# Kernel tuning notes

Hardware: AMD Instinct MI355X
Metric: run time of the kernel (lower is better)

Reference implementation:

```python
import jax, jax.numpy as jnp
import numpy as np

R_CUT = 10.0  # init arg r_cut


def _per_mol(pos, T, eneg, node_attrs, an, q_tot, eidx, hardness, cov_radii):
    # pos [N,3], T [N,E], eneg [N], node_attrs [N,num_el], an [N] int,
    # q_tot scalar, eidx [2,E] int
    N = pos.shape[0]
    E = T.shape[1]
    dtype = pos.dtype
    sqrt_pi = jnp.sqrt(jnp.pi).astype(dtype)
    sqrt_2 = jnp.sqrt(2.0).astype(dtype)
    eye = jnp.eye(N, dtype=dtype)
    # pairwise distances; +eye makes the (masked-out) diagonal sqrt-safe
    diff = pos[:, None, :] - pos[None, :, :]
    d = jnp.sqrt(jnp.sum(diff * diff, axis=-1) + eye)  # [N,N]
    r = cov_radii[an]                                   # [N]
    sigma = r * r
    gamma = jnp.sqrt(sigma[:, None] + sigma[None, :])   # [N,N]
    diag_vals = hardness[jnp.argmax(node_attrs, axis=-1)] + 1.0 / (sqrt_pi * r)
    A = jax.scipy.special.erf(d / (sqrt_2 * gamma)) / d * (1.0 - eye) + jnp.diag(diag_vals)
    # per-edge cutoff diagonal: 1/cos(pi*r/(2*r_cut)) - 1
    e0, e1 = eidx[0], eidx[1]
    edge_d = jnp.sqrt(jnp.sum((pos[e0] - pos[e1]) ** 2, axis=-1))  # [E]
    cut = 1.0 / jnp.cos(jnp.pi * edge_d / (2.0 * R_CUT)) - 1.0
    Ap = T.T @ A @ T + jnp.diag(cut)                    # [E,E]
    # augment with charge-conservation row/col of ones
    ones_col = jnp.ones((E, 1), dtype=dtype)
    ones_row = jnp.ones((1, E + 1), dtype=dtype)
    Aaug = jnp.concatenate([jnp.concatenate([Ap, ones_col], axis=1), ones_row], axis=0)
    b = jnp.concatenate([-(T.T @ eneg), q_tot[None]])   # [E+1]
    x = jnp.linalg.solve(Aaug, b)[:-1]                  # [E] split charges
    return T @ x                                        # [N] atomic partial charges


def setup_inputs() -> dict:
    key = jax.random.key(0)
    B, N, E, NUM_EL, NZ = 256, 64, 512, 10, 119
    ks = jax.random.split(key, 10)
    positions = jax.random.normal(ks[0], (B, N, 3), dtype=jnp.float32)
    T = jax.random.normal(ks[1], (B, N, E), dtype=jnp.float32)
    eneg = jax.random.normal(ks[2], (B, N), dtype=jnp.float32)
    node_attrs = jax.random.normal(ks[3], (B, N, NUM_EL), dtype=jnp.float32)
    total_charge = jax.random.normal(ks[4], (B,), dtype=jnp.float32)
    atomic_numbers = jax.random.randint(ks[5], (B, N), 1, 100)
    e0 = jax.random.randint(ks[6], (B, E), 0, N)
    off = jax.random.randint(ks[7], (B, E), 1, N)
    edge_index = jnp.stack([e0, (e0 + off) % N], axis=1)  # [B,2,E], distinct endpoints
    hardness = jax.random.uniform(ks[8], (NUM_EL,), dtype=jnp.float32)
    cov_radii = 0.3 + 2.2 * jax.random.uniform(ks[9], (NZ,), dtype=jnp.float32)
    p = jnp.zeros((1,), dtype=jnp.float32)  # only used for .device in torch
    return dict(positions=positions, T=T, eneg=eneg, node_attrs=node_attrs,
                total_charge=total_charge, p=p, hardness=hardness,
                cov_radii=cov_radii, atomic_numbers=atomic_numbers,
                edge_index=edge_index)


def reference(positions, T, eneg, node_attrs, total_charge, p, hardness,
              cov_radii, atomic_numbers, edge_index):
    charges = jax.vmap(_per_mol, in_axes=(0, 0, 0, 0, 0, 0, 0, None, None))(
        positions, T, eneg, node_attrs, atomic_numbers, total_charge,
        edge_index, hardness, cov_radii)  # [B,N]
    return charges.reshape(-1)  # concat over molecules, as in the torch loop
```

## Files before the change

kernel.cpp:

```cpp
#include <hip/hip_runtime.h>
#include <math.h>

#define SQRT_PI 1.7724538509055160273
#define SQRT_2  1.4142135623730950488
#define PI_OVER_2RC 0.15707963267948966

typedef double dbl4 __attribute__((ext_vector_type(4)));


__device__ __forceinline__ double bcast64(double v, int lane) {
    union { double d; unsigned int u[2]; } a, r;
    a.d = v;
    r.u[0] = __builtin_amdgcn_readlane(a.u[0], lane);
    r.u[1] = __builtin_amdgcn_readlane(a.u[1], lane);
    return r.d;
}

__device__ __forceinline__ double a_entry(int i, int j, const double* posd,
                                          const double* sig, const double* dg) {
    if (i == j) return dg[i];
    double dx = posd[3*i+0]-posd[3*j+0];
    double dy = posd[3*i+1]-posd[3*j+1];
    double dz = posd[3*i+2]-posd[3*j+2];
    double d  = sqrt(dx*dx+dy*dy+dz*dz);
    double g  = sqrt(sig[i]+sig[j]);
    return erf(d/(SQRT_2*g))/d;
}

__device__ __forceinline__ dbl4 mfma64(int cS, double xv, double yv, dbl4 acc) {
    return cS ? __builtin_amdgcn_mfma_f64_16x16x4f64(yv, xv, acc, 0, 0, 0)
              : __builtin_amdgcn_mfma_f64_16x16x4f64(xv, yv, acc, 0, 0, 0);
}

__global__ __launch_bounds__(64)
void k0_probe(double* __restrict__ fl)
{
    const int l = threadIdx.x;
    const int kl = l >> 4, ml = l & 15;
    const double af1 = (double)(l + 1),  bf1 = (double)(l + 65);
    const double af2 = (double)(1 + ((l*7 + 3) % 61));
    const double bf2 = (double)(2 + ((l*13 + 5) % 53));
    dbl4 c1 = {0.0,0.0,0.0,0.0}, c2 = {0.0,0.0,0.0,0.0};
    c1 = __builtin_amdgcn_mfma_f64_16x16x4f64(af1, bf1, c1, 0, 0, 0);
    c2 = __builtin_amdgcn_mfma_f64_16x16x4f64(af2, bf2, c2, 0, 0, 0);
    int best = -1;
    for (int h = 0; h < 32; ++h) {
        if (best >= 0) break;
        const int cS = h >> 4, cA = (h >> 3) & 1, cB = (h >> 2) & 1, cD = h & 3;
        bool ok = true;
        #pragma unroll
        for (int r = 0; r < 4; ++r) {
            int row, col;
            const int v0 = 4*kl + r, v1 = kl + 4*r;
            if (cD == 0)      { row = v0; col = ml; }
            else if (cD == 1) { row = v1; col = ml; }
            else if (cD == 2) { row = ml; col = v0; }
            else              { row = ml; col = v1; }
            double r1 = 0.0, r2 = 0.0;
            #pragma unroll
            for (int k = 0; k < 4; ++k) {
                const int la = cA ? (row*4 + k) : (row + 16*k);
                const int lb = cB ? (col*4 + k) : (col + 16*k);
                if (cS == 0) {
                    r1 += (double)(la + 1) * (double)(lb + 65);
                    r2 += (double)(1 + ((la*7+3) % 61)) * (double)(2 + ((lb*13+5) % 53));
                } else {
                    r1 += (double)(lb + 1) * (double)(la + 65);
                    r2 += (double)(1 + ((lb*7+3) % 61)) * (double)(2 + ((la*13+5) % 53));
                }
            }
            if (c1[r] != r1 || c2[r] != r2) ok = false;
        }
        if (__ballot(ok) == ~0ull) best = h;
    }
    if (l == 0) {
        fl[0] = (best >= 0) ? 1.0 : 0.0;
        fl[1] = (double)((best >= 0) ? (best >> 4)      : 0);
        fl[2] = (double)((best >= 0) ? ((best >> 3) & 1) : 0);
        fl[3] = (double)((best >= 0) ? ((best >> 2) & 1) : 0);
        fl[4] = (double)((best >= 0) ? (best & 3)        : 0);
    }
}

__global__ __launch_bounds__(1024)
void k_fused(const float* __restrict__ pos, const float* __restrict__ T,
             const int* __restrict__ eidx, const float* __restrict__ nattr,
             const float* __restrict__ eneg, const float* __restrict__ qtot,
             const float* __restrict__ hard, const float* __restrict__ covr,
             const int* __restrict__ an, const double* __restrict__ flq,
             float* __restrict__ outp)
{
    const int m = blockIdx.x, tid = threadIdx.x;
    const int jl = tid & 63;
    const int rg = tid >> 6;
    const int kl = jl >> 4, ml = jl & 15;

    __shared__ double R[2*64*66];
    __shared__ double AB[64*65];
    __shared__ double w_sl[512];
    __shared__ double posd[192], sig_s[64], dg_s[64], eneg_s[64];
    __shared__ double t0a_s[64], t0b_s[64], ga_s[64], gb_s[64];
    __shared__ double ua_s[64], ub_s[64], sa_s[64], sb_s[64];
    __shared__ double dinv_s[64], dvec_s[64];
    __shared__ double lam_sh, sw_sh;

    double* const Ta = R;
    double* const Tb = R + 64*66;
    double* const SB = R;
    double* const Pm = R + 64*66;

    const int cS = (int)flq[1], cA = (int)flq[2], cB = (int)flq[3], cD = (int)flq[4];
    const int aRow = cA ? (jl >> 2) : ml;
    const int aK   = cA ? (jl & 3)  : kl;
    const int bRow = cB ? (jl >> 2) : ml;
    const int bK   = cB ? (jl & 3)  : kl;
    int drow[4], dcol[4];
    #pragma unroll
    for (int r = 0; r < 4; ++r) {
        const int v0 = 4*kl + r, v1 = kl + 4*r;
        if (cD == 0)      { drow[r] = v0; dcol[r] = ml; }
        else if (cD == 1) { drow[r] = v1; dcol[r] = ml; }
        else if (cD == 2) { drow[r] = ml; dcol[r] = v0; }
        else              { drow[r] = ml; dcol[r] = v1; }
    }

    const float* Tm = T + (size_t)m*64*512;
    const int srow = tid >> 4, sc4 = (tid & 15) * 4;

    float4 v = *(const float4*)&Tm[srow*512 + sc4];

    if (tid < 64) {
        posd[3*tid+0] = (double)pos[(m*64+tid)*3+0];
        posd[3*tid+1] = (double)pos[(m*64+tid)*3+1];
        posd[3*tid+2] = (double)pos[(m*64+tid)*3+2];
        double r = (double)covr[an[m*64+tid]];
        sig_s[tid] = r*r;
        const float* np_ = nattr + (size_t)(m*64+tid)*10;
        float best = np_[0]; int bi = 0;
        #pragma unroll
        for (int k = 1; k < 10; ++k) { float vv = np_[k]; if (vv > best) { best = vv; bi = k; } }
        dg_s[tid] = (double)hard[bi] + 1.0/(SQRT_PI*r);
    } else if (tid < 128) {
        int ll = tid - 64;
        eneg_s[ll] = (double)eneg[m*64 + ll];
    }
    __syncthreads();

    if (tid < 512) {
        const int a0 = eidx[(size_t)m*1024 + tid];
        const int a1 = eidx[(size_t)m*1024 + 512 + tid];
        double dx = posd[3*a0+0]-posd[3*a1+0];
        double dy = posd[3*a0+1]-posd[3*a1+1];
        double dz = posd[3*a0+2]-posd[3*a1+2];
        double d  = sqrt(dx*dx+dy*dy+dz*dz);
        w_sl[tid] = 1.0 / (1.0/cos(PI_OVER_2RC*d) - 1.0);
    }
    __syncthreads();

    if (tid < 64) {
        double s = 0.0;
        #pragma unroll
        for (int c = 0; c < 8; ++c) s += w_sl[c*64 + tid];
        #pragma unroll
        for (int off = 32; off > 0; off >>= 1) s += __shfl_down(s, off);
        if (tid == 0) sw_sh = s;
    }

    const int tp = rg >> 2, tq = rg & 3;
    const double* ta_b = &Ta[(size_t)(tp*16 + aRow)*66 + aK];
    const double* tb_b = &Tb[(size_t)(tq*16 + bRow)*66 + bK];
    dbl4 vacc = {0.0, 0.0, 0.0, 0.0};
    double t0b_p = 0.0;
    double areg[4];

    #pragma unroll
    for (int cc = 0; cc < 8; ++cc) {
        __syncthreads();
        const double w0 = w_sl[cc*64 + sc4+0];
        const double w1 = w_sl[cc*64 + sc4+1];
        const double w2 = w_sl[cc*64 + sc4+2];
        const double w3 = w_sl[cc*64 + sc4+3];
        const double d0 = (double)v.x, d1 = (double)v.y;
        const double d2 = (double)v.z, d3 = (double)v.w;
        {
            double2 p0; p0.x = d0; p0.y = d1;
            double2 p1; p1.x = d2; p1.y = d3;
            *(double2*)&Ta[srow*66 + sc4]     = p0;
            *(double2*)&Ta[srow*66 + sc4 + 2] = p1;
            double2 q0; q0.x = w0*d0; q0.y = w1*d1;
            double2 q1; q1.x = w2*d2; q1.y = w3*d3;
            *(double2*)&Tb[srow*66 + sc4]     = q0;
            *(double2*)&Tb[srow*66 + sc4 + 2] = q1;
        }
        t0b_p += d0*w0 + d1*w1 + d2*w2 + d3*w3;
        if (cc < 7) v = *(const float4*)&Tm[srow*512 + (cc+1)*64 + sc4];
        __syncthreads();
        if (cc < 4) {
            const int i = rg + 16*cc;
            double av = a_entry(i, jl, posd, sig_s, dg_s);
            areg[cc] = av;
            AB[i*65 + jl] = av;
        }
        #pragma unroll
        for (int kk = 0; kk < 16; ++kk)
            vacc = mfma64(cS, ta_b[kk*4], tb_b[kk*4], vacc);
    }
    __syncthreads();

    #pragma unroll
    for (int r = 0; r < 4; ++r)
        SB[(tp*16 + drow[r])*66 + tq*16 + dcol[r]] = vacc[r];
    {
        double t = t0b_p;
        t += __shfl_down(t, 8, 16);
        t += __shfl_down(t, 4, 16);
        t += __shfl_down(t, 2, 16);
        t += __shfl_down(t, 1, 16);
        if ((tid & 15) == 0) t0b_s[tid >> 4] = t;
    }
    __syncthreads();

    {
        const int c16 = tid & 15, row16 = tid >> 4;
        double a = 0.0;
        #pragma unroll
        for (int kk = 0; kk < 4; ++kk)
            a += SB[row16*66 + 4*c16 + kk] * eneg_s[4*c16 + kk];
        a += __shfl_down(a, 8, 16);
        a += __shfl_down(a, 4, 16);
        a += __shfl_down(a, 2, 16);
        a += __shfl_down(a, 1, 16);
        if (c16 == 0) t0a_s[row16] = -a;
    }
    __syncthreads();

    {
        double ra[4], rb[4];
        const double ta = t0a_s[jl], tb = t0b_s[jl];
        #pragma unroll
        for (int p = 0; p < 4; ++p) { ra[p] = areg[p]*ta; rb[p] = areg[p]*tb; }
        #pragma unroll
        for (int off = 32; off > 0; off >>= 1) {
            #pragma unroll
            for (int p = 0; p < 4; ++p) {
                ra[p] += __shfl_down(ra[p], off);
                rb[p] += __shfl_down(rb[p], off);
            }
        }
        if (jl == 0) {
            #pragma unroll
            for (int p = 0; p < 4; ++p) { ga_s[rg+16*p] = ra[p]; gb_s[rg+16*p] = rb[p]; }
        }
    }
    __syncthreads();

    {
        const double* xb = &AB[(size_t)(tp*16 + aRow)*65 + aK];
        const double* yb = &SB[(size_t)bK*66 + tq*16 + bRow];
        dbl4 pacc = {0.0, 0.0, 0.0, 0.0};
        #pragma unroll
        for (int kk = 0; kk < 16; ++kk)
            pacc = mfma64(cS, xb[kk*4], yb[kk*264], pacc);
        #pragma unroll
        for (int r = 0; r < 4; ++r)
            Pm[(tp*16 + drow[r])*66 + tq*16 + dcol[r]] = pacc[r];
    }
    __syncthreads();

    {
        dbl4 macc;
        #pragma unroll
        for (int r = 0; r < 4; ++r)
            macc[r] = AB[(tp*16 + drow[r])*65 + tq*16 + dcol[r]];
        const double* xb = &Pm[(size_t)(tp*16 + aRow)*66 + aK];
        const double* yb = &AB[(size_t)bK*65 + tq*16 + bRow];
        #pragma unroll
        for (int kk = 0; kk < 16; ++kk)
            macc = mfma64(cS, xb[kk*4], yb[kk*260], macc);
        __syncthreads();
        #pragma unroll
        for (int r = 0; r < 4; ++r)
            AB[(tp*16 + drow[r])*65 + tq*16 + dcol[r]] = macc[r];
    }
    __syncthreads();

    for (int pb = 0; pb < 4; ++pb) {
        const int kb = pb*16;
        if (tid < 64) {
            const int i = tid;
            double pr[16];
            #pragma unroll
            for (int c = 0; c < 16; ++c) pr[c] = AB[i*65 + kb + c];
            #pragma unroll
            for (int c = 0; c < 16; ++c) {
                const int k = kb + c;
                const double Dk = bcast64(pr[c], k);
                const double di = 1.0 / Dk;
                if (i == k) { dinv_s[k] = di; dvec_s[k] = Dk; }
                const double lik = pr[c] * di;
                #pragma unroll
                for (int j = c+1; j < 16; ++j) {
                    const double mkj = bcast64(pr[j], k);
                    if (i > k) pr[j] -= lik * mkj;
                }
                if (i > k) pr[c] = lik;
            }
            #pragma unroll
            for (int c = 0; c < 16; ++c) AB[i*65 + kb + c] = pr[c];
        }
        __syncthreads();
        const int lim = kb + 16;
        if (lim < 64) {
            double tacc[4] = {0.0, 0.0, 0.0, 0.0};
            #pragma unroll 4
            for (int c = 0; c < 16; ++c) {
                double lbv = AB[jl*65 + kb + c] * dvec_s[kb + c];
                #pragma unroll
                for (int p = 0; p < 4; ++p)
                    tacc[p] += AB[(rg+16*p)*65 + kb + c] * lbv;
            }
            if (jl >= lim) {
                #pragma unroll
                for (int p = 0; p < 4; ++p) {
                    int i = rg + 16*p;
                    if (i >= lim) AB[i*65 + jl] -= tacc[p];
                }
            }
        }
        __syncthreads();
    }

    if (tid < 64) {
        const int i = tid;
        double ha = ga_s[i], hb = gb_s[i];
        #pragma unroll
        for (int j = 0; j < 63; ++j) {
            double xa = bcast64(ha, j), xb = bcast64(hb, j);
            double lij = (i > j) ? AB[i*65+j] : 0.0;
            ha -= lij*xa; hb -= lij*xb;
        }
        double di = dinv_s[i];
        ha *= di; hb *= di;
        #pragma unroll
        for (int j = 63; j > 0; --j) {
            double xa = bcast64(ha, j), xb = bcast64(hb, j);
            double lji = (i < j) ? AB[j*65+i] : 0.0;
            ha -= lji*xa; hb -= lji*xb;
        }
        ua_s[i] = ha; ub_s[i] = hb;
    }
    __syncthreads();

    {
        double ra[4], rb[4];
        const double uaj = ua_s[jl], ubj = ub_s[jl];
        #pragma unroll
        for (int p = 0; p < 4; ++p) { ra[p] = areg[p]*uaj; rb[p] = areg[p]*ubj; }
        #pragma unroll
        for (int off = 32; off > 0; off >>= 1) {
            #pragma unroll
            for (int p = 0; p < 4; ++p) {
                ra[p] += __shfl_down(ra[p], off);
                rb[p] += __shfl_down(rb[p], off);
            }
        }
        if (jl == 0) {
            #pragma unroll
            for (int p = 0; p < 4; ++p) {
                sa_s[rg + 16*p] = ra[p];
                sb_s[rg + 16*p] = rb[p];
            }
        }
    }
    __syncthreads();

    if (tid < 64) {
        double d1 = (eneg_s[tid] + sa_s[tid]) * t0b_s[tid];
        double d2 = sb_s[tid] * t0b_s[tid];
        #pragma unroll
        for (int off = 32; off > 0; off >>= 1) {
            d1 += __shfl_down(d1, off);
            d2 += __shfl_down(d2, off);
        }
        if (tid == 0) {
            double sY = -d1;
            double sZ = sw_sh - d2;
            lam_sh = ((double)qtot[m] - sY) / (1.0 - sZ);
        }
    }
    __syncthreads();
    if (tid < 64)
        outp[m*64 + tid] = (float)(ua_s[tid] - lam_sh*ub_s[tid]);
}

extern "C" void kernel_launch(void* const* d_in, const int* in_sizes, int n_in,
                              void* d_out, int out_size, void* d_ws, size_t ws_size,
                              hipStream_t stream) {
    const float* pos  = (const float*)d_in[0];
    const float* T    = (const float*)d_in[1];
    const float* eneg = (const float*)d_in[2];
    const float* nat  = (const float*)d_in[3];
    const float* qt   = (const float*)d_in[4];
    const float* hard = (const float*)d_in[6];
    const float* covr = (const float*)d_in[7];
    const int*   an   = (const int*)d_in[8];
    const int*   eidx = (const int*)d_in[9];
    float* outp = (float*)d_out;
    (void)n_in; (void)out_size; (void)ws_size;

    const int B = in_sizes[4];
    double* ws = (double*)d_ws;

    k0_probe<<<dim3(1), dim3(64), 0, stream>>>(ws);
    k_fused<<<dim3(B), dim3(1024), 0, stream>>>(pos, T, eidx, nat, eneg, qt,
                                                hard, covr, an, ws, outp);
}
```

Measured before the change: 169.1 us.

## Fuse MFMA layout probe, exploit Gram symmetry, and software-pipeline MFMA operand loads

Removes the separate probe kernel and runs the MFMA lane-layout detection inside each block, in parallel across four waves while other waves load per-atom data. The T^T·W·T Gram product is now computed only for its 10 upper-triangular 16x16 tiles. Waves are assigned to split the k-range of those tiles, with mirrored writes and a second accumulation pass. MFMA operand loads are double-buffered in registers, and a couple of barriers are merged or removed. This adds an extra sync and shared-memory read-modify-write, plus redundant probe work in every block.

```diff
diff --git a/kernel.cpp b/kernel.cpp
--- a/kernel.cpp
+++ b/kernel.cpp
@@ -6,7 +6,6 @@
 #define PI_OVER_2RC 0.15707963267948966
 
 typedef double dbl4 __attribute__((ext_vector_type(4)));
-
 
 __device__ __forceinline__ double bcast64(double v, int lane) {
     union { double d; unsigned int u[2]; } a, r;
@@ -32,63 +31,12 @@
               : __builtin_amdgcn_mfma_f64_16x16x4f64(xv, yv, acc, 0, 0, 0);
 }
 
-__global__ __launch_bounds__(64)
-void k0_probe(double* __restrict__ fl)
-{
-    const int l = threadIdx.x;
-    const int kl = l >> 4, ml = l & 15;
-    const double af1 = (double)(l + 1),  bf1 = (double)(l + 65);
-    const double af2 = (double)(1 + ((l*7 + 3) % 61));
-    const double bf2 = (double)(2 + ((l*13 + 5) % 53));
-    dbl4 c1 = {0.0,0.0,0.0,0.0}, c2 = {0.0,0.0,0.0,0.0};
-    c1 = __builtin_amdgcn_mfma_f64_16x16x4f64(af1, bf1, c1, 0, 0, 0);
-    c2 = __builtin_amdgcn_mfma_f64_16x16x4f64(af2, bf2, c2, 0, 0, 0);
-    int best = -1;
-    for (int h = 0; h < 32; ++h) {
-        if (best >= 0) break;
-        const int cS = h >> 4, cA = (h >> 3) & 1, cB = (h >> 2) & 1, cD = h & 3;
-        bool ok = true;
-        #pragma unroll
-        for (int r = 0; r < 4; ++r) {
-            int row, col;
-            const int v0 = 4*kl + r, v1 = kl + 4*r;
-            if (cD == 0)      { row = v0; col = ml; }
-            else if (cD == 1) { row = v1; col = ml; }
-            else if (cD == 2) { row = ml; col = v0; }
-            else              { row = ml; col = v1; }
-            double r1 = 0.0, r2 = 0.0;
-            #pragma unroll
-            for (int k = 0; k < 4; ++k) {
-                const int la = cA ? (row*4 + k) : (row + 16*k);
-                const int lb = cB ? (col*4 + k) : (col + 16*k);
-                if (cS == 0) {
-                    r1 += (double)(la + 1) * (double)(lb + 65);
-                    r2 += (double)(1 + ((la*7+3) % 61)) * (double)(2 + ((lb*13+5) % 53));
-                } else {
-                    r1 += (double)(lb + 1) * (double)(la + 65);
-                    r2 += (double)(1 + ((lb*7+3) % 61)) * (double)(2 + ((la*13+5) % 53));
-                }
-            }
-            if (c1[r] != r1 || c2[r] != r2) ok = false;
-        }
-        if (__ballot(ok) == ~0ull) best = h;
-    }
-    if (l == 0) {
-        fl[0] = (best >= 0) ? 1.0 : 0.0;
-        fl[1] = (double)((best >= 0) ? (best >> 4)      : 0);
-        fl[2] = (double)((best >= 0) ? ((best >> 3) & 1) : 0);
-        fl[3] = (double)((best >= 0) ? ((best >> 2) & 1) : 0);
-        fl[4] = (double)((best >= 0) ? (best & 3)        : 0);
-    }
-}
-
-__global__ __launch_bounds__(1024)
+__global__ __launch_bounds__(1024, 4)
 void k_fused(const float* __restrict__ pos, const float* __restrict__ T,
              const int* __restrict__ eidx, const float* __restrict__ nattr,
              const float* __restrict__ eneg, const float* __restrict__ qtot,
              const float* __restrict__ hard, const float* __restrict__ covr,
-             const int* __restrict__ an, const double* __restrict__ flq,
-             float* __restrict__ outp)
+             const int* __restrict__ an, float* __restrict__ outp)
 {
     const int m = blockIdx.x, tid = threadIdx.x;
     const int jl = tid & 63;
@@ -103,13 +51,77 @@
     __shared__ double ua_s[64], ub_s[64], sa_s[64], sb_s[64];
     __shared__ double dinv_s[64], dvec_s[64];
     __shared__ double lam_sh, sw_sh;
+    __shared__ int fl_w[4];
 
     double* const Ta = R;
     double* const Tb = R + 64*66;
     double* const SB = R;
     double* const Pm = R + 64*66;
 
-    const int cS = (int)flq[1], cA = (int)flq[2], cB = (int)flq[3], cD = (int)flq[4];
+    const float* Tm = T + (size_t)m*64*512;
+    const int srow = tid >> 4, sc4 = (tid & 15) * 4;
+
+    float4 v = *(const float4*)&Tm[srow*512 + sc4];
+
+    if (rg < 4) {
+        const double af1 = (double)(jl + 1),  bf1 = (double)(jl + 65);
+        const double af2 = (double)(1 + ((jl*7 + 3) % 61));
+        const double bf2 = (double)(2 + ((jl*13 + 5) % 53));
+        dbl4 c1 = {0.0,0.0,0.0,0.0}, c2 = {0.0,0.0,0.0,0.0};
+        c1 = __builtin_amdgcn_mfma_f64_16x16x4f64(af1, bf1, c1, 0, 0, 0);
+        c2 = __builtin_amdgcn_mfma_f64_16x16x4f64(af2, bf2, c2, 0, 0, 0);
+        int myh = -1;
+        for (int hh = 0; hh < 8; ++hh) {
+            const int h = rg*8 + hh;
+            const int pS = h >> 4, pA = (h >> 3) & 1, pB = (h >> 2) & 1, pD = h & 3;
+            bool ok = true;
+            #pragma unroll
+            for (int r = 0; r < 4; ++r) {
+                int row, col;
+                const int v0 = 4*kl + r, v1 = kl + 4*r;
+                if (pD == 0)      { row = v0; col = ml; }
+                else if (pD == 1) { row = v1; col = ml; }
+                else if (pD == 2) { row = ml; col = v0; }
+                else              { row = ml; col = v1; }
+                double r1 = 0.0, r2 = 0.0;
+                #pragma unroll
+                for (int k = 0; k < 4; ++k) {
+                    const int la = pA ? (row*4 + k) : (row + 16*k);
+                    const int lb = pB ? (col*4 + k) : (col + 16*k);
+                    if (pS == 0) {
+                        r1 += (double)(la + 1) * (double)(lb + 65);
+                        r2 += (double)(1 + ((la*7+3) % 61)) * (double)(2 + ((lb*13+5) % 53));
+                    } else {
+                        r1 += (double)(lb + 1) * (double)(la + 65);
+                        r2 += (double)(1 + ((lb*7+3) % 61)) * (double)(2 + ((la*13+5) % 53));
+                    }
+                }
+                if (c1[r] != r1 || c2[r] != r2) ok = false;
+            }
+            if (__ballot(ok) == ~0ull) myh = h;
+        }
+        if (jl == 0) fl_w[rg] = myh;
+    } else if (tid >= 256 && tid < 320) {
+        const int at = tid - 256;
+        posd[3*at+0] = (double)pos[(m*64+at)*3+0];
+        posd[3*at+1] = (double)pos[(m*64+at)*3+1];
+        posd[3*at+2] = (double)pos[(m*64+at)*3+2];
+        double r = (double)covr[an[m*64+at]];
+        sig_s[at] = r*r;
+        const float* np_ = nattr + (size_t)(m*64+at)*10;
+        float best = np_[0]; int bi = 0;
+        #pragma unroll
+        for (int k = 1; k < 10; ++k) { float vv = np_[k]; if (vv > best) { best = vv; bi = k; } }
+        dg_s[at] = (double)hard[bi] + 1.0/(SQRT_PI*r);
+    } else if (tid >= 320 && tid < 384) {
+        const int at = tid - 320;
+        eneg_s[at] = (double)eneg[m*64 + at];
+    }
+    __syncthreads();
+
+    int hbest = max(max(fl_w[0], fl_w[1]), max(fl_w[2], fl_w[3]));
+    if (hbest < 0) hbest = 1;
+    const int cS = hbest >> 4, cA = (hbest >> 3) & 1, cB = (hbest >> 2) & 1, cD = hbest & 3;
     const int aRow = cA ? (jl >> 2) : ml;
     const int aK   = cA ? (jl & 3)  : kl;
     const int bRow = cB ? (jl >> 2) : ml;
@@ -124,28 +136,6 @@
         else              { drow[r] = ml; dcol[r] = v1; }
     }
 
-    const float* Tm = T + (size_t)m*64*512;
-    const int srow = tid >> 4, sc4 = (tid & 15) * 4;
-
-    float4 v = *(const float4*)&Tm[srow*512 + sc4];
-
-    if (tid < 64) {
-        posd[3*tid+0] = (double)pos[(m*64+tid)*3+0];
-        posd[3*tid+1] = (double)pos[(m*64+tid)*3+1];
-        posd[3*tid+2] = (double)pos[(m*64+tid)*3+2];
-        double r = (double)covr[an[m*64+tid]];
-        sig_s[tid] = r*r;
-        const float* np_ = nattr + (size_t)(m*64+tid)*10;
-        float best = np_[0]; int bi = 0;
-        #pragma unroll
-        for (int k = 1; k < 10; ++k) { float vv = np_[k]; if (vv > best) { best = vv; bi = k; } }
-        dg_s[tid] = (double)hard[bi] + 1.0/(SQRT_PI*r);
-    } else if (tid < 128) {
-        int ll = tid - 64;
-        eneg_s[ll] = (double)eneg[m*64 + ll];
-    }
-    __syncthreads();
-
     if (tid < 512) {
         const int a0 = eidx[(size_t)m*1024 + tid];
         const int a1 = eidx[(size_t)m*1024 + 512 + tid];
@@ -155,18 +145,13 @@
         double d  = sqrt(dx*dx+dy*dy+dz*dz);
         w_sl[tid] = 1.0 / (1.0/cos(PI_OVER_2RC*d) - 1.0);
     }
-    __syncthreads();
-
-    if (tid < 64) {
-        double s = 0.0;
-        #pragma unroll
-        for (int c = 0; c < 8; ++c) s += w_sl[c*64 + tid];
-        #pragma unroll
-        for (int off = 32; off > 0; off >>= 1) s += __shfl_down(s, off);
-        if (tid == 0) sw_sh = s;
-    }
-
-    const int tp = rg >> 2, tq = rg & 3;
+
+    const int TP_[10] = {0,1,1,2,2,2,3,3,3,3};
+    const int TQ_[10] = {0,0,1,0,1,2,0,1,2,3};
+    const int WT[16] = {0,4,4,5,5,1,6,6,7,7,2,8,8,9,9,3};
+    const int WM[16] = {0,1,2,1,2,0,1,2,1,2,0,1,2,1,2,0};
+    const int myt = WT[rg], wm = WM[rg];
+    const int tp = TP_[myt], tq = TQ_[myt];
     const double* ta_b = &Ta[(size_t)(tp*16 + aRow)*66 + aK];
     const double* tb_b = &Tb[(size_t)(tq*16 + bRow)*66 + bK];
     dbl4 vacc = {0.0, 0.0, 0.0, 0.0};
@@ -195,21 +180,55 @@
         t0b_p += d0*w0 + d1*w1 + d2*w2 + d3*w3;
         if (cc < 7) v = *(const float4*)&Tm[srow*512 + (cc+1)*64 + sc4];
         __syncthreads();
+        if (cc == 0 && tid >= 128 && tid < 192) {
+            const int ll = tid - 128;
+            double s = 0.0;
+            #pragma unroll
+            for (int c = 0; c < 8; ++c) s += w_sl[c*64 + ll];
+            #pragma unroll
+            for (int off = 32; off > 0; off >>= 1) s += __shfl_down(s, off);
+            if (ll == 0) sw_sh = s;
+        }
         if (cc < 4) {
             const int i = rg + 16*cc;
             double av = a_entry(i, jl, posd, sig_s, dg_s);
             areg[cc] = av;
             AB[i*65 + jl] = av;
         }
-        #pragma unroll
-        for (int kk = 0; kk < 16; ++kk)
-            vacc = mfma64(cS, ta_b[kk*4], tb_b[kk*4], vacc);
-    }
-    __syncthreads();
-
-    #pragma unroll
-    for (int r = 0; r < 4; ++r)
-        SB[(tp*16 + drow[r])*66 + tq*16 + dcol[r]] = vacc[r];
+        const bool act = (wm == 0) || (wm == 1 ? ((cc & 1) == 0) : ((cc & 1) == 1));
+        if (act) {
+            double xc[4], yc[4];
+            #pragma unroll
+            for (int q = 0; q < 4; ++q) { xc[q] = ta_b[q*4]; yc[q] = tb_b[q*4]; }
+            #pragma unroll
+            for (int kb = 0; kb < 4; ++kb) {
+                double xn[4], yn[4];
+                if (kb < 3) {
+                    #pragma unroll
+                    for (int q = 0; q < 4; ++q) {
+                        xn[q] = ta_b[(kb*4+4+q)*4];
+                        yn[q] = tb_b[(kb*4+4+q)*4];
+                    }
+                }
+                #pragma unroll
+                for (int q = 0; q < 4; ++q) vacc = mfma64(cS, xc[q], yc[q], vacc);
+                if (kb < 3) {
+                    #pragma unroll
+                    for (int q = 0; q < 4; ++q) { xc[q] = xn[q]; yc[q] = yn[q]; }
+                }
+            }
+        }
+    }
+    __syncthreads();
+
+    if (wm != 2) {
+        #pragma unroll
+        for (int r = 0; r < 4; ++r) {
+            const int ri = tp*16 + drow[r], cj = tq*16 + dcol[r];
+            SB[ri*66 + cj] = vacc[r];
+            if (tp != tq) SB[cj*66 + ri] = vacc[r];
+        }
+    }
     {
         double t = t0b_p;
         t += __shfl_down(t, 8, 16);
@@ -219,8 +238,45 @@
         if ((tid & 15) == 0) t0b_s[tid >> 4] = t;
     }
     __syncthreads();
-
+    if (wm == 2) {
+        #pragma unroll
+        for (int r = 0; r < 4; ++r) {
+            const int ri = tp*16 + drow[r], cj = tq*16 + dcol[r];
+            const double vv = vacc[r];
+            SB[ri*66 + cj] += vv;
+            if (tp != tq) SB[cj*66 + ri] += vv;
+        }
+    }
+    __syncthreads();
+
+    const int ti = rg >> 2, tj = rg & 3;
     {
+        const double* xb = &AB[(size_t)(ti*16 + aRow)*65 + aK];
+        const double* yb = &SB[(size_t)bK*66 + tj*16 + bRow];
+        dbl4 pacc = {0.0, 0.0, 0.0, 0.0};
+        double xc[4], yc[4];
+        #pragma unroll
+        for (int q = 0; q < 4; ++q) { xc[q] = xb[q*4]; yc[q] = yb[q*264]; }
+        #pragma unroll
+        for (int kb = 0; kb < 4; ++kb) {
+            double xn[4], yn[4];
+            if (kb < 3) {
+                #pragma unroll
+                for (int q = 0; q < 4; ++q) {
+                    xn[q] = xb[(kb*4+4+q)*4];
+                    yn[q] = yb[(size_t)(kb*4+4+q)*264];
+                }
+            }
+            #pragma unroll
+            for (int q = 0; q < 4; ++q) pacc = mfma64(cS, xc[q], yc[q], pacc);
+            if (kb < 3) {
+                #pragma unroll
+                for (int q = 0; q < 4; ++q) { xc[q] = xn[q]; yc[q] = yn[q]; }
+            }
+        }
+        #pragma unroll
+        for (int r = 0; r < 4; ++r)
+            Pm[(ti*16 + drow[r])*66 + tj*16 + dcol[r]] = pacc[r];
         const int c16 = tid & 15, row16 = tid >> 4;
         double a = 0.0;
         #pragma unroll
@@ -235,52 +291,54 @@
     __syncthreads();
 
     {
-        double ra[4], rb[4];
-        const double ta = t0a_s[jl], tb = t0b_s[jl];
-        #pragma unroll
-        for (int p = 0; p < 4; ++p) { ra[p] = areg[p]*ta; rb[p] = areg[p]*tb; }
-        #pragma unroll
-        for (int off = 32; off > 0; off >>= 1) {
-            #pragma unroll
-            for (int p = 0; p < 4; ++p) {
-                ra[p] += __shfl_down(ra[p], off);
-                rb[p] += __shfl_down(rb[p], off);
-            }
-        }
-        if (jl == 0) {
-            #pragma unroll
-            for (int p = 0; p < 4; ++p) { ga_s[rg+16*p] = ra[p]; gb_s[rg+16*p] = rb[p]; }
-        }
-    }
-    __syncthreads();
-
-    {
-        const double* xb = &AB[(size_t)(tp*16 + aRow)*65 + aK];
-        const double* yb = &SB[(size_t)bK*66 + tq*16 + bRow];
-        dbl4 pacc = {0.0, 0.0, 0.0, 0.0};
-        #pragma unroll
-        for (int kk = 0; kk < 16; ++kk)
-            pacc = mfma64(cS, xb[kk*4], yb[kk*264], pacc);
+        dbl4 macc;
         #pragma unroll
         for (int r = 0; r < 4; ++r)
-            Pm[(tp*16 + drow[r])*66 + tq*16 + dcol[r]] = pacc[r];
-    }
-    __syncthreads();
-
-    {
-        dbl4 macc;
+            macc[r] = AB[(ti*16 + drow[r])*65 + tj*16 + dcol[r]];
+        const double* xb = &Pm[(size_t)(ti*16 + aRow)*66 + aK];
+        const double* yb = &AB[(size_t)bK*65 + tj*16 + bRow];
+        double xc[4], yc[4];
+        #pragma unroll
+        for (int q = 0; q < 4; ++q) { xc[q] = xb[q*4]; yc[q] = yb[q*260]; }
+        #pragma unroll
+        for (int kb = 0; kb < 4; ++kb) {
+            double xn[4], yn[4];
+            if (kb < 3) {
+                #pragma unroll
+                for (int q = 0; q < 4; ++q) {
+                    xn[q] = xb[(kb*4+4+q)*4];
+                    yn[q] = yb[(size_t)(kb*4+4+q)*260];
+                }
+            }
+            #pragma unroll
+            for (int q = 0; q < 4; ++q) macc = mfma64(cS, xc[q], yc[q], macc);
+            if (kb < 3) {
+                #pragma unroll
+                for (int q = 0; q < 4; ++q) { xc[q] = xn[q]; yc[q] = yn[q]; }
+            }
+        }
+        {
+            double ra[4], rb[4];
+            const double ta = t0a_s[jl], tb = t0b_s[jl];
+            #pragma unroll
+            for (int p = 0; p < 4; ++p) { ra[p] = areg[p]*ta; rb[p] = areg[p]*tb; }
+            #pragma unroll
+            for (int off = 32; off > 0; off >>= 1) {
+                #pragma unroll
+                for (int p = 0; p < 4; ++p) {
+                    ra[p] += __shfl_down(ra[p], off);
+                    rb[p] += __shfl_down(rb[p], off);
+                }
+            }
+            if (jl == 0) {
+                #pragma unroll
+                for (int p = 0; p < 4; ++p) { ga_s[rg+16*p] = ra[p]; gb_s[rg+16*p] = rb[p]; }
+            }
+        }
+        __syncthreads();
         #pragma unroll
         for (int r = 0; r < 4; ++r)
-            macc[r] = AB[(tp*16 + drow[r])*65 + tq*16 + dcol[r]];
-        const double* xb = &Pm[(size_t)(tp*16 + aRow)*66 + aK];
-        const double* yb = &AB[(size_t)bK*65 + tq*16 + bRow];
-        #pragma unroll
-        for (int kk = 0; kk < 16; ++kk)
-            macc = mfma64(cS, xb[kk*4], yb[kk*260], macc);
-        __syncthreads();
-        #pragma unroll
-        for (int r = 0; r < 4; ++r)
-            AB[(tp*16 + drow[r])*65 + tq*16 + dcol[r]] = macc[r];
+            AB[(ti*16 + drow[r])*65 + tj*16 + dcol[r]] = macc[r];
     }
     __syncthreads();
 
@@ -406,12 +464,9 @@
     const int*   an   = (const int*)d_in[8];
     const int*   eidx = (const int*)d_in[9];
     float* outp = (float*)d_out;
-    (void)n_in; (void)out_size; (void)ws_size;
+    (void)n_in; (void)out_size; (void)d_ws; (void)ws_size;
 
     const int B = in_sizes[4];
-    double* ws = (double*)d_ws;
-
-    k0_probe<<<dim3(1), dim3(64), 0, stream>>>(ws);
     k_fused<<<dim3(B), dim3(1024), 0, stream>>>(pos, T, eidx, nat, eneg, qt,
-                                                hard, covr, an, ws, outp);
+                                                hard, covr, an, outp);
 }
```

After: 190.8 us. 1.13x slower.

## Exploit symmetry of T^T A T tile product and split triangular solves across warps

Applied to the files above, without the earlier changes.

Computes only the upper-triangular 16x16 tiles of the symmetric T-product. Off-diagonal tiles are split across two waves, one taking even and one taking odd K-chunks, then summed and mirrored into SB. This removes a barrier by folding the weight-sum reduction into the main loop, and runs the two forward/back substitutions on two separate waves instead of interleaving them in one. The cost is extra accumulate passes and barriers, and uneven wave load on the diagonal tiles.

```diff
diff --git a/kernel.cpp b/kernel.cpp
--- a/kernel.cpp
+++ b/kernel.cpp
@@ -155,18 +155,26 @@
         double d  = sqrt(dx*dx+dy*dy+dz*dz);
         w_sl[tid] = 1.0 / (1.0/cos(PI_OVER_2RC*d) - 1.0);
     }
-    __syncthreads();
-
-    if (tid < 64) {
-        double s = 0.0;
-        #pragma unroll
-        for (int c = 0; c < 8; ++c) s += w_sl[c*64 + tid];
-        #pragma unroll
-        for (int off = 32; off > 0; off >>= 1) s += __shfl_down(s, off);
-        if (tid == 0) sw_sh = s;
-    }
-
-    const int tp = rg >> 2, tq = rg & 3;
+
+    int tp, tq, wm;
+    switch (rg) {
+        case 0:  tp=0; tq=0; wm=0; break;
+        case 5:  tp=1; tq=1; wm=0; break;
+        case 10: tp=2; tq=2; wm=0; break;
+        case 15: tp=3; tq=3; wm=0; break;
+        case 1:  tp=1; tq=0; wm=1; break;
+        case 2:  tp=1; tq=0; wm=2; break;
+        case 3:  tp=2; tq=0; wm=1; break;
+        case 4:  tp=2; tq=0; wm=2; break;
+        case 6:  tp=2; tq=1; wm=1; break;
+        case 7:  tp=2; tq=1; wm=2; break;
+        case 8:  tp=3; tq=0; wm=1; break;
+        case 9:  tp=3; tq=0; wm=2; break;
+        case 11: tp=3; tq=1; wm=1; break;
+        case 12: tp=3; tq=1; wm=2; break;
+        case 13: tp=3; tq=2; wm=1; break;
+        default: tp=3; tq=2; wm=2; break;
+    }
     const double* ta_b = &Ta[(size_t)(tp*16 + aRow)*66 + aK];
     const double* tb_b = &Tb[(size_t)(tq*16 + bRow)*66 + bK];
     dbl4 vacc = {0.0, 0.0, 0.0, 0.0};
@@ -193,23 +201,40 @@
             *(double2*)&Tb[srow*66 + sc4 + 2] = q1;
         }
         t0b_p += d0*w0 + d1*w1 + d2*w2 + d3*w3;
+        __syncthreads();
         if (cc < 7) v = *(const float4*)&Tm[srow*512 + (cc+1)*64 + sc4];
-        __syncthreads();
+        if (cc == 0 && tid >= 128 && tid < 192) {
+            const int ll = tid - 128;
+            double s = 0.0;
+            #pragma unroll
+            for (int c = 0; c < 8; ++c) s += w_sl[c*64 + ll];
+            #pragma unroll
+            for (int off = 32; off > 0; off >>= 1) s += __shfl_down(s, off);
+            if (ll == 0) sw_sh = s;
+        }
         if (cc < 4) {
             const int i = rg + 16*cc;
             double av = a_entry(i, jl, posd, sig_s, dg_s);
             areg[cc] = av;
             AB[i*65 + jl] = av;
         }
-        #pragma unroll
-        for (int kk = 0; kk < 16; ++kk)
-            vacc = mfma64(cS, ta_b[kk*4], tb_b[kk*4], vacc);
-    }
-    __syncthreads();
-
-    #pragma unroll
-    for (int r = 0; r < 4; ++r)
-        SB[(tp*16 + drow[r])*66 + tq*16 + dcol[r]] = vacc[r];
+        const bool act = (wm == 0) || (wm == 1 ? ((cc & 1) == 0) : ((cc & 1) == 1));
+        if (act) {
+            #pragma unroll
+            for (int kk = 0; kk < 16; ++kk)
+                vacc = mfma64(cS, ta_b[kk*4], tb_b[kk*4], vacc);
+        }
+    }
+    __syncthreads();
+
+    if (wm != 2) {
+        #pragma unroll
+        for (int r = 0; r < 4; ++r) {
+            const int ri = tp*16 + drow[r], cj = tq*16 + dcol[r];
+            SB[ri*66 + cj] = vacc[r];
+            if (tp != tq) SB[cj*66 + ri] = vacc[r];
+        }
+    }
     {
         double t = t0b_p;
         t += __shfl_down(t, 8, 16);
@@ -217,6 +242,16 @@
         t += __shfl_down(t, 2, 16);
         t += __shfl_down(t, 1, 16);
         if ((tid & 15) == 0) t0b_s[tid >> 4] = t;
+    }
+    __syncthreads();
+    if (wm == 2) {
+        #pragma unroll
+        for (int r = 0; r < 4; ++r) {
+            const int ri = tp*16 + drow[r], cj = tq*16 + dcol[r];
+            const double vv = vacc[r];
+            SB[ri*66 + cj] += vv;
+            if (tp != tq) SB[cj*66 + ri] += vv;
+        }
     }
     __syncthreads();
 
@@ -254,16 +289,17 @@
     }
     __syncthreads();
 
-    {
-        const double* xb = &AB[(size_t)(tp*16 + aRow)*65 + aK];
-        const double* yb = &SB[(size_t)bK*66 + tq*16 + bRow];
+    const int ti = rg >> 2, tj = rg & 3;
+    {
+        const double* xb = &AB[(size_t)(ti*16 + aRow)*65 + aK];
+        const double* yb = &SB[(size_t)bK*66 + tj*16 + bRow];
         dbl4 pacc = {0.0, 0.0, 0.0, 0.0};
         #pragma unroll
         for (int kk = 0; kk < 16; ++kk)
             pacc = mfma64(cS, xb[kk*4], yb[kk*264], pacc);
         #pragma unroll
         for (int r = 0; r < 4; ++r)
-            Pm[(tp*16 + drow[r])*66 + tq*16 + dcol[r]] = pacc[r];
+            Pm[(ti*16 + drow[r])*66 + tj*16 + dcol[r]] = pacc[r];
     }
     __syncthreads();
 
@@ -271,16 +307,16 @@
         dbl4 macc;
         #pragma unroll
         for (int r = 0; r < 4; ++r)
-            macc[r] = AB[(tp*16 + drow[r])*65 + tq*16 + dcol[r]];
-        const double* xb = &Pm[(size_t)(tp*16 + aRow)*66 + aK];
-        const double* yb = &AB[(size_t)bK*65 + tq*16 + bRow];
+            macc[r] = AB[(ti*16 + drow[r])*65 + tj*16 + dcol[r]];
+        const double* xb = &Pm[(size_t)(ti*16 + aRow)*66 + aK];
+        const double* yb = &AB[(size_t)bK*65 + tj*16 + bRow];
         #pragma unroll
         for (int kk = 0; kk < 16; ++kk)
             macc = mfma64(cS, xb[kk*4], yb[kk*260], macc);
         __syncthreads();
         #pragma unroll
         for (int r = 0; r < 4; ++r)
-            AB[(tp*16 + drow[r])*65 + tq*16 + dcol[r]] = macc[r];
+            AB[(ti*16 + drow[r])*65 + tj*16 + dcol[r]] = macc[r];
     }
     __syncthreads();
 
@@ -330,24 +366,23 @@
         __syncthreads();
     }
 
-    if (tid < 64) {
-        const int i = tid;
-        double ha = ga_s[i], hb = gb_s[i];
+    if (tid < 128) {
+        const int i = jl;
+        double h = (rg == 0) ? ga_s[i] : gb_s[i];
         #pragma unroll
         for (int j = 0; j < 63; ++j) {
-            double xa = bcast64(ha, j), xb = bcast64(hb, j);
+            double x = bcast64(h, j);
             double lij = (i > j) ? AB[i*65+j] : 0.0;
-            ha -= lij*xa; hb -= lij*xb;
-        }
-        double di = dinv_s[i];
-        ha *= di; hb *= di;
+            h -= lij*x;
+        }
+        h *= dinv_s[i];
         #pragma unroll
         for (int j = 63; j > 0; --j) {
-            double xa = bcast64(ha, j), xb = bcast64(hb, j);
+            double x = bcast64(h, j);
             double lji = (i < j) ? AB[j*65+i] : 0.0;
-            ha -= lji*xa; hb -= lji*xb;
-        }
-        ua_s[i] = ha; ub_s[i] = hb;
+            h -= lji*x;
+        }
+        if (rg == 0) ua_s[i] = h; else ub_s[i] = h;
     }
     __syncthreads();
 
```

Measured after the change: 162.6 us. 3.8% less time.
